# Kernel optimization log

Measured on AMD Instinct MI355X. Metric: run time of the kernel, lower is better.

The kernel has to match this reference:

```python
import jax, jax.numpy as jnp
import numpy as np

N, D0, D1, D2 = 8192, 512, 256, 64


def setup_inputs() -> dict:
    key = jax.random.key(0)
    k1, k2, k3, k4 = jax.random.split(key, 4)
    xi = jax.random.normal(k1, (N, D0), dtype=jnp.float32)
    # graph filter ~ row-normalized adjacency: nonnegative, entries O(1/N)
    filter_matrix = jax.random.uniform(k2, (N, N), dtype=jnp.float32) * (2.0 / N)
    b1 = np.sqrt(6.0 / (D0 + D1))
    b2 = np.sqrt(6.0 / (D1 + D2))
    w1 = jax.random.uniform(k3, (D0, D1), dtype=jnp.float32, minval=-b1, maxval=b1)
    w2 = jax.random.uniform(k4, (D1, D2), dtype=jnp.float32, minval=-b2, maxval=b2)
    return {"xi": xi, "filter_matrix": filter_matrix, "w1": w1, "w2": w2}


def reference(xi, filter_matrix, w1, w2):
    # two GCN layers: F @ (X @ W)
    h = jax.nn.relu(filter_matrix @ (xi @ w1))          # [N, D1]
    emb = filter_matrix @ (h @ w2)                       # [N, D2]
    # pairwise squared Euclidean distances between rows of emb -> [N, N]
    sq = jnp.sum(emb * emb, axis=1)                      # [N]
    dists = jnp.maximum(sq[:, None] + sq[None, :] - 2.0 * (emb @ emb.T), 0.0)
    recons_w = jax.nn.softmax(-dists, axis=1)            # row softmax of negative distances
    return emb, recons_w + 1e-10
```

## Files before the change

kernel.cpp:

```cpp
#include <hip/hip_runtime.h>

typedef short s16x8 __attribute__((ext_vector_type(8)));
typedef float f32x4 __attribute__((ext_vector_type(4)));
typedef unsigned int u32;

#define DEV static __device__ __forceinline__

DEV unsigned short f2bf(float x){
  u32 u = __builtin_bit_cast(u32, x);
  return (unsigned short)((u + 0x7FFFu + ((u >> 16) & 1u)) >> 16);
}
DEV float bf2f(unsigned short h){ u32 u = ((u32)h) << 16; return __builtin_bit_cast(float, u); }
DEV u32 pack2(float a, float b){ return (u32)f2bf(a) | ((u32)f2bf(b) << 16); }

DEV void gld16(const void* g, void* l){
  __builtin_amdgcn_global_load_lds((const __attribute__((address_space(1))) u32*)g,
                                   (__attribute__((address_space(3))) u32*)l, 16, 0, 0);
}

template<int N> DEV void vmwait(){
  static_assert(N>=0 && N<=8, "vmcnt range");
  if constexpr (N==0) asm volatile("s_waitcnt vmcnt(0)" ::: "memory");
  else if constexpr (N==1) asm volatile("s_waitcnt vmcnt(1)" ::: "memory");
  else if constexpr (N==2) asm volatile("s_waitcnt vmcnt(2)" ::: "memory");
  else if constexpr (N==3) asm volatile("s_waitcnt vmcnt(3)" ::: "memory");
  else if constexpr (N==4) asm volatile("s_waitcnt vmcnt(4)" ::: "memory");
  else if constexpr (N==5) asm volatile("s_waitcnt vmcnt(5)" ::: "memory");
  else if constexpr (N==6) asm volatile("s_waitcnt vmcnt(6)" ::: "memory");
  else if constexpr (N==7) asm volatile("s_waitcnt vmcnt(7)" ::: "memory");
  else                     asm volatile("s_waitcnt vmcnt(8)" ::: "memory");
}
DEV void pipebar(){
  __builtin_amdgcn_sched_barrier(0);
  __builtin_amdgcn_s_barrier();
  __builtin_amdgcn_sched_barrier(0);
}

DEV void cvt_body(const float* __restrict__ src, unsigned short* __restrict__ dst,
                  long n4, int bid, int nblocks){
  long i = (long)bid*256 + threadIdx.x;
  long stride = (long)nblocks*256;
  for (; i + 3*stride < n4; i += 4*stride){
    float4 v0 = ((const float4*)src)[i];
    float4 v1 = ((const float4*)src)[i+stride];
    float4 v2 = ((const float4*)src)[i+2*stride];
    float4 v3 = ((const float4*)src)[i+3*stride];
    int2 p0{(int)pack2(v0.x,v0.y),(int)pack2(v0.z,v0.w)};
    int2 p1{(int)pack2(v1.x,v1.y),(int)pack2(v1.z,v1.w)};
    int2 p2{(int)pack2(v2.x,v2.y),(int)pack2(v2.z,v2.w)};
    int2 p3{(int)pack2(v3.x,v3.y),(int)pack2(v3.z,v3.w)};
    ((int2*)dst)[i] = p0;
    ((int2*)dst)[i+stride] = p1;
    ((int2*)dst)[i+2*stride] = p2;
    ((int2*)dst)[i+3*stride] = p3;
  }
  for (; i < n4; i += stride){
    float4 v = ((const float4*)src)[i];
    int2 p{(int)pack2(v.x,v.y),(int)pack2(v.z,v.w)};
    ((int2*)dst)[i] = p;
  }
}

__global__ void k_cvt(const float* __restrict__ src, unsigned short* __restrict__ dst, long n4){
  cvt_body(src, dst, n4, blockIdx.x, gridDim.x);
}

__global__ __launch_bounds__(256)
void k_misc(const float* __restrict__ w1, const float* __restrict__ w2,
            unsigned short* __restrict__ w1t, unsigned short* __restrict__ w2t,
            const float* __restrict__ xi, unsigned short* __restrict__ xib){
  int bid = blockIdx.x;
  if (bid < 576){
    int idx = bid*256 + threadIdx.x;
    if (idx < 512*256){ int r=idx/256, c=idx%256; w1t[(size_t)c*512 + r] = f2bf(w1[idx]); }
    else { int j = idx - 512*256; if (j < 256*64){ int r=j/64, c=j%64; w2t[(size_t)c*256 + r] = f2bf(w2[j]); } }
  } else {
    cvt_body(xi, xib, (long)8192*512/4, bid-576, 512);
  }
}

template<int ROWS,int BK,int THREADS>
DEV void stage_lds(const unsigned short* __restrict__ src, int row0, int ld,
                   int kk, char* lds, int tid){
  constexpr int SLOTS = BK/8, SLM = SLOTS-1, RPC = 64/SLOTS;
  constexpr int RSH = (SLOTS==4) ? 1 : 0;
  constexpr int NCH = ROWS*BK*2/1024;
  constexpr int NW = THREADS/64, NI = NCH/NW;
  static_assert(NI*NW==NCH, "chunk exact");
  const int lane = tid & 63, wid = tid >> 6;
  #pragma unroll
  for (int i=0;i<NI;i++){
    int c = i*NW + wid;
    int r = c*RPC + lane/SLOTS;
    int s = lane & SLM;
    int ks = s ^ ((r>>RSH)&SLM);
    gld16(src + (size_t)(row0+r)*ld + kk + ks*8, lds + c*1024);
  }
}

template<int BM,int BN,int BK,int WR,int WC,bool PART>
DEV void gemm_body(const unsigned short* __restrict__ A, const unsigned short* __restrict__ B,
                   void* __restrict__ Cp, int lda, int ldb, int ldc, int kchunk,
                   long pstride, char* smem, int bx, int by, int bz)
{
  constexpr int THREADS = WR*WC*64;
  constexpr int ROWB = BK*2, SLOTS = BK/8, SLM = SLOTS-1;
  constexpr int RSH = (SLOTS==4) ? 1 : 0;
  constexpr int TBYTES = (BM+BN)*ROWB;
  constexpr int WM = BM/WR, WN = BN/WC;
  constexpr int FM = WM/16, FN = WN/16, KS = BK/32;
  constexpr int LA = BM*ROWB/1024/(THREADS/64);
  constexpr int LB = BN*ROWB/1024/(THREADS/64);
  constexpr int L  = LA + LB;

  const int tid = threadIdx.x, lane = tid & 63;
  const int wid = tid >> 6, wrr = wid / WC, wcc = wid % WC;
  const int m0 = by * BM, n0 = bx * BN;
  const int kbeg = bz * kchunk, nk = kchunk / BK;

  f32x4 acc[FM][FN];
  f32x4 z4 = {0.f,0.f,0.f,0.f};
  #pragma unroll
  for (int m=0;m<FM;m++)
    #pragma unroll
    for (int n=0;n<FN;n++) acc[m][n] = z4;

  auto stage = [&](int kk, char* buf){
    stage_lds<BM,BK,THREADS>(A, m0, lda, kk, buf, tid);
    stage_lds<BN,BK,THREADS>(B, n0, ldb, kk, buf + BM*ROWB, tid);
  };
  auto compute = [&](const char* buf){
    const char* bA = buf;
    const char* bB = buf + BM*ROWB;
    #pragma unroll
    for (int ks=0;ks<KS;ks++){
      s16x8 av[FM], bv[FN];
      #pragma unroll
      for (int m=0;m<FM;m++){
        int r = wrr*WM + m*16 + (lane&15);
        int s = (ks*4 + (lane>>4)) ^ ((r>>RSH)&SLM);
        av[m] = *(const s16x8*)(bA + r*ROWB + s*16);
      }
      #pragma unroll
      for (int n=0;n<FN;n++){
        int r = wcc*WN + n*16 + (lane&15);
        int s = (ks*4 + (lane>>4)) ^ ((r>>RSH)&SLM);
        bv[n] = *(const s16x8*)(bB + r*ROWB + s*16);
      }
      #pragma unroll
      for (int m=0;m<FM;m++)
        #pragma unroll
        for (int n=0;n<FN;n++)
          acc[m][n] = __builtin_amdgcn_mfma_f32_16x16x32_bf16(av[m], bv[n], acc[m][n], 0, 0, 0);
    }
  };

  char* bc  = smem;
  char* bn_ = smem + TBYTES;
  char* bf_ = smem + 2*TBYTES;

  stage(kbeg, bc);
  stage(kbeg + BK, bn_);

  for (int t=0; t<nk; t++){
    if (t+1 < nk) vmwait<L>();
    else          vmwait<0>();
    pipebar();
    if (t+2 < nk) stage(kbeg + (t+2)*BK, bf_);
    compute(bc);
    pipebar();
    char* tmp = bc; bc = bn_; bn_ = bf_; bf_ = tmp;
  }

  if constexpr (PART) {
    float* Cf = (float*)Cp + (size_t)bz * pstride;
    #pragma unroll
    for (int m=0;m<FM;m++)
      #pragma unroll
      for (int n=0;n<FN;n++)
        #pragma unroll
        for (int r=0;r<4;r++){
          int row = m0 + wrr*WM + m*16 + (lane>>4)*4 + r;
          int col = n0 + wcc*WN + n*16 + (lane&15);
          Cf[(size_t)row*ldc + col] = acc[m][n][r];
        }
  } else {
    unsigned short* Ch = (unsigned short*)Cp;
    #pragma unroll
    for (int m=0;m<FM;m++)
      #pragma unroll
      for (int n=0;n<FN;n++)
        #pragma unroll
        for (int r=0;r<4;r++){
          int row = m0 + wrr*WM + m*16 + (lane>>4)*4 + r;
          int col = n0 + wcc*WN + n*16 + (lane&15);
          Ch[(size_t)row*ldc + col] = f2bf(acc[m][n][r]);
        }
  }
}

template<int BM,int BN,int BK,int WR,int WC,bool PART>
__global__ __launch_bounds__(WR*WC*64, 4)
void k_gemm(const unsigned short* __restrict__ A, const unsigned short* __restrict__ B,
            void* __restrict__ Cp, int lda, int ldb, int ldc, int kchunk, long pstride)
{
  __shared__ char smem[3*(BM+BN)*BK*2];
  gemm_body<BM,BN,BK,WR,WC,PART>(A, B, Cp, lda, ldb, ldc, kchunk, pstride,
                                 smem, blockIdx.x, blockIdx.y, blockIdx.z);
}

__global__ void k_hred(const float* __restrict__ hp, unsigned short* __restrict__ h){
  const long N = (long)8192*256/4;
  long i = (long)blockIdx.x*256 + threadIdx.x;
  if (i >= N) return;
  float4 s = ((const float4*)hp)[i];
  #pragma unroll
  for (int z=1; z<8; z++){
    float4 v = ((const float4*)(hp + (size_t)z*8192*256))[i];
    s.x+=v.x; s.y+=v.y; s.z+=v.z; s.w+=v.w;
  }
  int2 p;
  p.x = (int)pack2(fmaxf(s.x,0.f), fmaxf(s.y,0.f));
  p.y = (int)pack2(fmaxf(s.z,0.f), fmaxf(s.w,0.f));
  ((int2*)h)[i] = p;
}

__global__ void k_emb_fin(const float* __restrict__ ep, float* __restrict__ emb_out,
                          unsigned short* __restrict__ embb, float* __restrict__ sq){
  int idx = blockIdx.x*256 + threadIdx.x;
  float v = 0.f;
  #pragma unroll
  for (int z=0; z<8; z++) v += ep[(size_t)z*8192*64 + idx];
  emb_out[idx] = v;
  unsigned short ub = f2bf(v);
  embb[idx] = ub;
  float x = bf2f(ub);
  float s = x*x;
  #pragma unroll
  for (int off=32; off>0; off>>=1) s += __shfl_xor(s, off, 64);
  if ((threadIdx.x & 63)==0) sq[idx>>6] = s;
}

template<int PASS>
__global__ __launch_bounds__(256)
void k_dist(const unsigned short* __restrict__ embb, const float* __restrict__ sq,
            float* __restrict__ S, float* __restrict__ out)
{
  constexpr int ROWB = 128, SLM = 7;
  __shared__ char smem[2*128*128];
  char* bufA = smem;
  char* bufB = smem + 128*ROWB;
  const int tid=threadIdx.x, lane=tid&63, wid=tid>>6;
  const int wrr = wid>>1, wcc = wid&1;
  const int i0 = blockIdx.y*128, j0 = blockIdx.x*128;

  #pragma unroll
  for (int i=0;i<4;i++){
    int u = tid + i*256;
    int r = u>>3, c = u&7;
    int byte = r*ROWB + ((c^(r&SLM))*16);
    *(int4*)(bufA+byte) = *(const int4*)(embb + (size_t)(i0+r)*64 + c*8);
    *(int4*)(bufB+byte) = *(const int4*)(embb + (size_t)(j0+r)*64 + c*8);
  }
  __syncthreads();

  f32x4 acc[4][4];
  f32x4 z4 = {0.f,0.f,0.f,0.f};
  #pragma unroll
  for (int m=0;m<4;m++)
    #pragma unroll
    for (int n=0;n<4;n++) acc[m][n]=z4;

  #pragma unroll
  for (int ks=0;ks<2;ks++){
    s16x8 av[4], bv[4];
    #pragma unroll
    for (int m=0;m<4;m++){
      int r = wrr*64 + m*16 + (lane&15);
      int slot = (ks*4 + (lane>>4)) ^ (r&SLM);
      av[m] = *(const s16x8*)(bufA + r*ROWB + slot*16);
    }
    #pragma unroll
    for (int n=0;n<4;n++){
      int r = wcc*64 + n*16 + (lane&15);
      int slot = (ks*4 + (lane>>4)) ^ (r&SLM);
      bv[n] = *(const s16x8*)(bufB + r*ROWB + slot*16);
    }
    #pragma unroll
    for (int m=0;m<4;m++)
      #pragma unroll
      for (int n=0;n<4;n++)
        acc[m][n] = __builtin_amdgcn_mfma_f32_16x16x32_bf16(av[m], bv[n], acc[m][n], 0, 0, 0);
  }

  float sqj[4];
  #pragma unroll
  for (int n=0;n<4;n++) sqj[n] = sq[j0 + wcc*64 + n*16 + (lane&15)];

  #pragma unroll
  for (int m=0;m<4;m++){
    #pragma unroll
    for (int r=0;r<4;r++){
      int row = i0 + wrr*64 + m*16 + (lane>>4)*4 + r;
      float sqi = sq[row];
      if constexpr (PASS==1){
        float v = 0.f;
        #pragma unroll
        for (int n=0;n<4;n++){
          float d = fmaxf(sqi + sqj[n] - 2.f*acc[m][n][r], 0.f);
          v += __expf(-d);
        }
        #pragma unroll
        for (int off=1; off<16; off<<=1) v += __shfl_xor(v, off, 64);
        if ((lane&15)==0) atomicAdd(S+row, v);
      } else {
        float inv = 1.0f / S[row];
        #pragma unroll
        for (int n=0;n<4;n++){
          int col = j0 + wcc*64 + n*16 + (lane&15);
          float d = fmaxf(sqi + sqj[n] - 2.f*acc[m][n][r], 0.f);
          out[(size_t)row*8192 + col] = __expf(-d)*inv + 1e-10f;
        }
      }
    }
  }
}

extern "C" void kernel_launch(void* const* d_in, const int* in_sizes, int n_in,
                              void* d_out, int out_size, void* d_ws, size_t ws_size,
                              hipStream_t stream)
{
  const float* xi = (const float*)d_in[0];
  const float* F  = (const float*)d_in[1];
  const float* w1 = (const float*)d_in[2];
  const float* w2 = (const float*)d_in[3];
  float* out = (float*)d_out;
  float* emb_out = out;
  float* recons  = out + (size_t)8192*64;

  unsigned short* Fb = (unsigned short*)recons;

  char* ws = (char*)d_ws;
  size_t off = 0;
  auto alloc = [&](size_t bytes)->char*{ char* p = ws + off; off += (bytes + 255) & ~(size_t)255; return p; };
  unsigned short* w1t  = (unsigned short*)alloc((size_t)256*512*2);
  unsigned short* w2t  = (unsigned short*)alloc((size_t)64*256*2);
  unsigned short* xib  = (unsigned short*)alloc((size_t)8192*512*2);
  unsigned short* t1t  = (unsigned short*)alloc((size_t)256*8192*2);
  unsigned short* t2t  = (unsigned short*)alloc((size_t)64*8192*2);
  unsigned short* h    = (unsigned short*)alloc((size_t)8192*256*2);
  unsigned short* embb = (unsigned short*)alloc((size_t)8192*64*2);
  float* sq     = (float*)alloc((size_t)8192*4);
  float* h_part = (float*)alloc((size_t)8*8192*256*4);
  float* e_part = (float*)alloc((size_t)8*8192*64*4);
  float* S      = (float*)alloc((size_t)8192*4);

  hipMemsetAsync(S, 0, (size_t)8192*4, stream);

  k_misc<<<dim3(1088),256,0,stream>>>(w1, w2, w1t, w2t, xi, xib);

  k_cvt<<<dim3(2048),256,0,stream>>>(F, Fb, (long)8192*8192/4);

  k_gemm<64,64,64,2,2,false><<<dim3(128,4,1),256,0,stream>>>(
      w1t, xib, t1t, 512, 512, 8192, 512, 0);

  k_gemm<128,256,32,2,4,true><<<dim3(1,64,8),512,0,stream>>>(
      Fb, t1t, h_part, 8192, 8192, 256, 1024, (long)8192*256);

  k_hred<<<dim3(2048),256,0,stream>>>(h_part, h);

  k_gemm<64,32,64,2,2,false><<<dim3(256,1,1),256,0,stream>>>(
      w2t, h, t2t, 256, 256, 8192, 256, 0);

  k_gemm<128,64,64,4,2,true><<<dim3(1,64,8),512,0,stream>>>(
      Fb, t2t, e_part, 8192, 8192, 64, 1024, (long)8192*64);

  k_emb_fin<<<dim3(8192*64/256),256,0,stream>>>(e_part, emb_out, embb, sq);

  k_dist<1><<<dim3(64,64),256,0,stream>>>(embb, sq, S, recons);
  k_dist<2><<<dim3(64,64),256,0,stream>>>(embb, sq, S, recons);
}
```

Baseline: 369.7 us.

## Merge conversion kernels, retile two GEMMs, replace global atomics with LDS partial sums

Folds the F-to-bf16 conversion into the weight/xi conversion kernel so one launch does all the streaming casts, and drops the memset. The first GEMM moves to 128x64 tiles and the F@t2 GEMM to 4 waves instead of 8. The softmax row-sum pass now accumulates in shared memory per block and writes per-column-block partials, which a new small kernel then reduces. This replaces contended global float atomics but adds a launch and a 2 MB partials buffer.

```diff
diff --git a/kernel.cpp b/kernel.cpp
--- a/kernel.cpp
+++ b/kernel.cpp
@@ -61,21 +61,20 @@
   }
 }
 
-__global__ void k_cvt(const float* __restrict__ src, unsigned short* __restrict__ dst, long n4){
-  cvt_body(src, dst, n4, blockIdx.x, gridDim.x);
-}
-
 __global__ __launch_bounds__(256)
-void k_misc(const float* __restrict__ w1, const float* __restrict__ w2,
-            unsigned short* __restrict__ w1t, unsigned short* __restrict__ w2t,
-            const float* __restrict__ xi, unsigned short* __restrict__ xib){
+void k_stream(const float* __restrict__ w1, const float* __restrict__ w2,
+              unsigned short* __restrict__ w1t, unsigned short* __restrict__ w2t,
+              const float* __restrict__ xi, unsigned short* __restrict__ xib,
+              const float* __restrict__ F, unsigned short* __restrict__ Fb){
   int bid = blockIdx.x;
   if (bid < 576){
     int idx = bid*256 + threadIdx.x;
     if (idx < 512*256){ int r=idx/256, c=idx%256; w1t[(size_t)c*512 + r] = f2bf(w1[idx]); }
     else { int j = idx - 512*256; if (j < 256*64){ int r=j/64, c=j%64; w2t[(size_t)c*256 + r] = f2bf(w2[j]); } }
+  } else if (bid < 1088){
+    cvt_body(xi, xib, (long)8192*512/4, bid-576, 512);
   } else {
-    cvt_body(xi, xib, (long)8192*512/4, bid-576, 512);
+    cvt_body(F, Fb, (long)8192*8192/4, bid-1088, 2048);
   }
 }
 
@@ -99,9 +98,9 @@
 }
 
 template<int BM,int BN,int BK,int WR,int WC,bool PART>
-DEV void gemm_body(const unsigned short* __restrict__ A, const unsigned short* __restrict__ B,
-                   void* __restrict__ Cp, int lda, int ldb, int ldc, int kchunk,
-                   long pstride, char* smem, int bx, int by, int bz)
+__global__ __launch_bounds__(WR*WC*64, 4)
+void k_gemm(const unsigned short* __restrict__ A, const unsigned short* __restrict__ B,
+            void* __restrict__ Cp, int lda, int ldb, int ldc, int kchunk, long pstride)
 {
   constexpr int THREADS = WR*WC*64;
   constexpr int ROWB = BK*2, SLOTS = BK/8, SLM = SLOTS-1;
@@ -113,10 +112,12 @@
   constexpr int LB = BN*ROWB/1024/(THREADS/64);
   constexpr int L  = LA + LB;
 
+  __shared__ char smem[3*TBYTES];
+
   const int tid = threadIdx.x, lane = tid & 63;
   const int wid = tid >> 6, wrr = wid / WC, wcc = wid % WC;
-  const int m0 = by * BM, n0 = bx * BN;
-  const int kbeg = bz * kchunk, nk = kchunk / BK;
+  const int m0 = blockIdx.y * BM, n0 = blockIdx.x * BN;
+  const int kbeg = blockIdx.z * kchunk, nk = kchunk / BK;
 
   f32x4 acc[FM][FN];
   f32x4 z4 = {0.f,0.f,0.f,0.f};
@@ -173,7 +174,7 @@
   }
 
   if constexpr (PART) {
-    float* Cf = (float*)Cp + (size_t)bz * pstride;
+    float* Cf = (float*)Cp + (size_t)blockIdx.z * pstride;
     #pragma unroll
     for (int m=0;m<FM;m++)
       #pragma unroll
@@ -199,16 +200,6 @@
   }
 }
 
-template<int BM,int BN,int BK,int WR,int WC,bool PART>
-__global__ __launch_bounds__(WR*WC*64, 4)
-void k_gemm(const unsigned short* __restrict__ A, const unsigned short* __restrict__ B,
-            void* __restrict__ Cp, int lda, int ldb, int ldc, int kchunk, long pstride)
-{
-  __shared__ char smem[3*(BM+BN)*BK*2];
-  gemm_body<BM,BN,BK,WR,WC,PART>(A, B, Cp, lda, ldb, ldc, kchunk, pstride,
-                                 smem, blockIdx.x, blockIdx.y, blockIdx.z);
-}
-
 __global__ void k_hred(const float* __restrict__ hp, unsigned short* __restrict__ h){
   const long N = (long)8192*256/4;
   long i = (long)blockIdx.x*256 + threadIdx.x;
@@ -244,15 +235,18 @@
 template<int PASS>
 __global__ __launch_bounds__(256)
 void k_dist(const unsigned short* __restrict__ embb, const float* __restrict__ sq,
-            float* __restrict__ S, float* __restrict__ out)
+            float* __restrict__ Spart, const float* __restrict__ S, float* __restrict__ out)
 {
   constexpr int ROWB = 128, SLM = 7;
   __shared__ char smem[2*128*128];
+  __shared__ float ldsS[128];
   char* bufA = smem;
   char* bufB = smem + 128*ROWB;
   const int tid=threadIdx.x, lane=tid&63, wid=tid>>6;
   const int wrr = wid>>1, wcc = wid&1;
   const int i0 = blockIdx.y*128, j0 = blockIdx.x*128;
+
+  if (PASS==1 && tid < 128) ldsS[tid] = 0.f;
 
   #pragma unroll
   for (int i=0;i<4;i++){
@@ -301,7 +295,8 @@
   for (int m=0;m<4;m++){
     #pragma unroll
     for (int r=0;r<4;r++){
-      int row = i0 + wrr*64 + m*16 + (lane>>4)*4 + r;
+      int rloc = wrr*64 + m*16 + (lane>>4)*4 + r;
+      int row  = i0 + rloc;
       float sqi = sq[row];
       if constexpr (PASS==1){
         float v = 0.f;
@@ -312,7 +307,7 @@
         }
         #pragma unroll
         for (int off=1; off<16; off<<=1) v += __shfl_xor(v, off, 64);
-        if ((lane&15)==0) atomicAdd(S+row, v);
+        if ((lane&15)==0) atomicAdd(&ldsS[rloc], v);
       } else {
         float inv = 1.0f / S[row];
         #pragma unroll
@@ -324,6 +319,19 @@
       }
     }
   }
+
+  if constexpr (PASS==1){
+    __syncthreads();
+    if (tid < 128) Spart[(size_t)blockIdx.x*8192 + i0 + tid] = ldsS[tid];
+  }
+}
+
+__global__ void k_sred(const float* __restrict__ Spart, float* __restrict__ S){
+  int i = blockIdx.x*256 + threadIdx.x;
+  float v = 0.f;
+  #pragma unroll
+  for (int b=0; b<64; b++) v += Spart[(size_t)b*8192 + i];
+  S[i] = v;
 }
 
 extern "C" void kernel_launch(void* const* d_in, const int* in_sizes, int n_in,
@@ -353,15 +361,12 @@
   float* sq     = (float*)alloc((size_t)8192*4);
   float* h_part = (float*)alloc((size_t)8*8192*256*4);
   float* e_part = (float*)alloc((size_t)8*8192*64*4);
+  float* Spart  = (float*)alloc((size_t)64*8192*4);
   float* S      = (float*)alloc((size_t)8192*4);
 
-  hipMemsetAsync(S, 0, (size_t)8192*4, stream);
-
-  k_misc<<<dim3(1088),256,0,stream>>>(w1, w2, w1t, w2t, xi, xib);
-
-  k_cvt<<<dim3(2048),256,0,stream>>>(F, Fb, (long)8192*8192/4);
-
-  k_gemm<64,64,64,2,2,false><<<dim3(128,4,1),256,0,stream>>>(
+  k_stream<<<dim3(3136),256,0,stream>>>(w1, w2, w1t, w2t, xi, xib, F, Fb);
+
+  k_gemm<128,64,64,2,2,false><<<dim3(128,2,1),256,0,stream>>>(
       w1t, xib, t1t, 512, 512, 8192, 512, 0);
 
   k_gemm<128,256,32,2,4,true><<<dim3(1,64,8),512,0,stream>>>(
@@ -372,11 +377,12 @@
   k_gemm<64,32,64,2,2,false><<<dim3(256,1,1),256,0,stream>>>(
       w2t, h, t2t, 256, 256, 8192, 256, 0);
 
-  k_gemm<128,64,64,4,2,true><<<dim3(1,64,8),512,0,stream>>>(
+  k_gemm<128,64,64,2,2,true><<<dim3(1,64,8),256,0,stream>>>(
       Fb, t2t, e_part, 8192, 8192, 64, 1024, (long)8192*64);
 
   k_emb_fin<<<dim3(8192*64/256),256,0,stream>>>(e_part, emb_out, embb, sq);
 
-  k_dist<1><<<dim3(64,64),256,0,stream>>>(embb, sq, S, recons);
-  k_dist<2><<<dim3(64,64),256,0,stream>>>(embb, sq, S, recons);
-}
+  k_dist<1><<<dim3(64,64),256,0,stream>>>(embb, sq, Spart, nullptr, recons);
+  k_sred<<<dim3(32),256,0,stream>>>(Spart, S);
+  k_dist<2><<<dim3(64,64),256,0,stream>>>(embb, sq, nullptr, S, recons);
+}
```

Measured after the change: 324.9 us, median of 2. 12.1% less time.
